# Kernel optimization log

Hardware: AMD Instinct MI355X
Metric: run time of the kernel (lower is better)

## Reference

```python
import jax, jax.numpy as jnp
import numpy as np

B, N, C, H = 2, 1024, 1024, 16
HD = C // H
PAST = 8192
CACHE_BUDGET = 4000
ANCHOR = 512            # anchor_token_count (first-frame tokens preserved)
IMP_W = 0.5             # importance_weight
SCALE = HD ** -0.5


def setup_inputs() -> dict:
    key = jax.random.key(0)
    ks = jax.random.split(key, 8)
    return {
        "x": jax.random.normal(ks[0], (B, N, C), jnp.float32),
        "past_k": jax.random.normal(ks[1], (B, H, PAST, HD), jnp.float32),
        "past_v": jax.random.normal(ks[2], (B, H, PAST, HD), jnp.float32),
        "importance_scores": jax.random.uniform(ks[3], (B, N), dtype=jnp.float32),
        "qkv_w": jax.random.normal(ks[4], (3 * C, C), jnp.float32) * 0.02,
        "qkv_b": jnp.zeros((3 * C,), jnp.float32),
        "proj_w": jax.random.normal(ks[5], (C, C), jnp.float32) * 0.02,
        "proj_b": jnp.zeros((C,), jnp.float32),
    }


def _eviction(k, v, imp):
    # k, v: [B, H, Ntot, D]; imp: [B, N_new]. Hybrid branch of Attention.eviction.
    Bb, Hh, Ntot, D = k.shape
    A = ANCHOR
    Nc = Ntot - A                      # candidates
    keep = CACHE_BUDGET - A            # num_to_keep_from_candidates
    n_old = Nc - N                     # old (past-frame) candidates
    anchor_k, cand_k = k[:, :, :A], k[:, :, A:]
    anchor_v, cand_v = v[:, :, :A], v[:, :, A:]
    # cosine-diversity baseline (F.normalize uses eps=1e-12)
    kn = cand_k / jnp.maximum(jnp.linalg.norm(cand_k, axis=-1, keepdims=True), 1e-12)
    mean_vec = kn.mean(axis=2, keepdims=True)              # [B,H,1,D]
    baseline = jnp.sum(kn * mean_vec, axis=-1)             # [B,H,Nc]
    div_avg = (1.0 - baseline).mean(axis=1)                # [B,Nc]
    old = div_avg[:, :n_old]
    old_n = (old - old.min(axis=-1, keepdims=True)) / (
        old.max(axis=-1, keepdims=True) - old.min(axis=-1, keepdims=True) + 1e-8)
    new_n = (imp - imp.min(axis=-1, keepdims=True)) / (
        imp.max(axis=-1, keepdims=True) - imp.min(axis=-1, keepdims=True) + 1e-8)
    combined = jnp.concatenate([(1.0 - IMP_W) * old_n, IMP_W * new_n], axis=-1)  # [B,Nc]
    _, idx = jax.lax.top_k(combined, keep)
    idx = jnp.sort(idx, axis=-1)                           # [B,keep]
    gidx = jnp.broadcast_to(idx[:, None, :, None], (Bb, Hh, keep, D))
    kept_k = jnp.take_along_axis(cand_k, gidx, axis=2)
    kept_v = jnp.take_along_axis(cand_v, gidx, axis=2)
    return (jnp.concatenate([anchor_k, kept_k], axis=2),
            jnp.concatenate([anchor_v, kept_v], axis=2))


def reference(x, past_k, past_v, importance_scores, qkv_w, qkv_b, proj_w, proj_b):
    # qkv projection -> [3, B, H, N, HD]
    qkv = (x @ qkv_w.T + qkv_b).reshape(B, N, 3, H, HD).transpose(2, 0, 3, 1, 4)
    q, k, v = qkv[0], qkv[1], qkv[2]
    # append to KV cache
    k = jnp.concatenate([past_k, k], axis=2)
    v = jnp.concatenate([past_v, v], axis=2)
    # KV-cache eviction (topk importance + cosine diversity + gather compaction)
    k, v = _eviction(k, v, importance_scores)              # [B,H,CACHE_BUDGET,HD]
    # scaled dot-product attention
    attn = jax.nn.softmax(jnp.einsum('bhqd,bhkd->bhqk', q, k) * SCALE, axis=-1)
    out = jnp.einsum('bhqk,bhkd->bhqd', attn, v)
    out = out.transpose(0, 2, 1, 3).reshape(B, N, C)
    return out @ proj_w.T + proj_b
```

## Files before the change

### kernel.cpp

```cpp
#include <hip/hip_runtime.h>
#include <hip/hip_bf16.h>

typedef unsigned short u16;
typedef unsigned int   u32;
typedef __attribute__((ext_vector_type(8)))  short v8s;
typedef __attribute__((ext_vector_type(4)))  float v4f;
typedef __attribute__((ext_vector_type(16))) float v16f;
typedef __attribute__((ext_vector_type(4)))  u32   v4u;
typedef __attribute__((ext_vector_type(2)))  u32   v2u;

#define B_      2
#define N_      1024
#define C_      1024
#define H_      16
#define BH_     32
#define PAST_   8192
#define BUDGET  4000
#define ANCHOR_ 512
#define NCAND   8704
#define NOLD    7680
#define KEEPN   3488
#define NSPLIT  4
#define QSCALE  0.18033688011112042f

__device__ __forceinline__ u16 f2bf(float f) {
    u32 u = __float_as_uint(f);
    u32 r = u + 0x7fffu + ((u >> 16) & 1u);
    return (u16)(r >> 16);
}
__device__ __forceinline__ float bf2f(u16 h) {
    return __uint_as_float(((u32)h) << 16);
}
__device__ __forceinline__ u32 pk2(float a, float b) {
    __hip_bfloat162 t = __float22bfloat162_rn(float2{a, b});
    u32 r; __builtin_memcpy(&r, &t, 4); return r;
}
__device__ __forceinline__ v8s mk8(u32 a, u32 b, u32 c, u32 d) {
    v4u t; t[0] = a; t[1] = b; t[2] = c; t[3] = d;
    return __builtin_bit_cast(v8s, t);
}

__global__ void prep(const float* __restrict__ x, const float* __restrict__ qw,
                     const float* __restrict__ pw, u16* __restrict__ xcat,
                     u16* __restrict__ wcat, u16* __restrict__ wpbf) {
    const int i = blockIdx.x * 256 + threadIdx.x;
    const int NX = 2048 * 1024, NW = 3072 * 1024;
    if (i < NX) {
        float v = x[i];
        u16 hi = f2bf(v); float lo = v - bf2f(hi);
        const int m = i >> 10, k = i & 1023;
        u16* p = xcat + (size_t)m * 3072 + k;
        p[0] = hi; p[1024] = hi; p[2048] = f2bf(lo);
    } else if (i < NX + NW) {
        const int j = i - NX;
        float v = qw[j];
        u16 hi = f2bf(v); float lo = v - bf2f(hi);
        const int n = j >> 10, k = j & 1023;
        u16* p = wcat + (size_t)n * 3072 + k;
        p[0] = hi; p[1024] = f2bf(lo); p[2048] = hi;
    } else {
        const int j = i - NX - NW;
        wpbf[j] = f2bf(pw[j]);
    }
}

__global__ __launch_bounds__(256) void gemm_qkv(
    const u16* __restrict__ A, const u16* __restrict__ Bm,
    const float* __restrict__ bias,
    u16* __restrict__ Qbf, float* __restrict__ Vnew, float* __restrict__ Kpart) {
    __shared__ u16 As[128 * 72];
    __shared__ u16 Bs[128 * 72];
    const int tid = threadIdx.x;
    const int l = tid & 63, w = tid >> 6;
    const int wm = w >> 1, wn = w & 1;
    const int bid = blockIdx.x;
    int tsel, by, bx, s;
    if (bid < 128)      { tsel = 0; by = bid >> 3; bx = bid & 7; s = 0; }
    else if (bid < 256) { int r = bid - 128; tsel = 2; by = r >> 3; bx = r & 7; s = 0; }
    else                { int r = bid - 256; s = r >> 7; r &= 127; tsel = 1; by = r >> 3; bx = r & 7; }
    const int ks = s * 1024;
    const int nbase = tsel * 1024 + bx * 128;

    v4f acc[4][4];
    #pragma unroll
    for (int a = 0; a < 4; ++a)
        #pragma unroll
        for (int b = 0; b < 4; ++b) { acc[a][b][0]=0.f; acc[a][b][1]=0.f; acc[a][b][2]=0.f; acc[a][b][3]=0.f; }

    const int srow = tid >> 1, shalf = tid & 1;
    const u16* pa = A  + ((size_t)(by * 128 + srow)) * 3072 + ks + shalf * 32;
    const u16* pb = Bm + ((size_t)(nbase + srow))    * 3072 + ks + shalf * 32;
    v4u ar[4], br[4];
    #pragma unroll
    for (int j = 0; j < 4; ++j) { ar[j] = *(const v4u*)(pa + j * 8); br[j] = *(const v4u*)(pb + j * 8); }

    for (int k0 = 0; k0 < 1024; k0 += 64) {
        #pragma unroll
        for (int j = 0; j < 4; ++j) {
            *(v4u*)(&As[srow * 72 + shalf * 32 + j * 8]) = ar[j];
            *(v4u*)(&Bs[srow * 72 + shalf * 32 + j * 8]) = br[j];
        }
        __syncthreads();
        if (k0 + 64 < 1024) {
            #pragma unroll
            for (int j = 0; j < 4; ++j) {
                ar[j] = *(const v4u*)(pa + (k0 + 64) + j * 8);
                br[j] = *(const v4u*)(pb + (k0 + 64) + j * 8);
            }
        }
        #pragma unroll
        for (int kc = 0; kc < 2; ++kc) {
            v8s af[4], bfr[4];
            #pragma unroll
            for (int mt = 0; mt < 4; ++mt)
                af[mt] = *(const v8s*)(&As[(wm * 64 + mt * 16 + (l & 15)) * 72 + kc * 32 + (l >> 4) * 8]);
            #pragma unroll
            for (int nt = 0; nt < 4; ++nt)
                bfr[nt] = *(const v8s*)(&Bs[(wn * 64 + nt * 16 + (l & 15)) * 72 + kc * 32 + (l >> 4) * 8]);
            #pragma unroll
            for (int mt = 0; mt < 4; ++mt)
                #pragma unroll
                for (int nt = 0; nt < 4; ++nt)
                    acc[mt][nt] = __builtin_amdgcn_mfma_f32_16x16x32_bf16(af[mt], bfr[nt], acc[mt][nt], 0, 0, 0);
        }
        __syncthreads();
    }
    #pragma unroll
    for (int nt = 0; nt < 4; ++nt) {
        const int nl = bx * 128 + wn * 64 + nt * 16 + (l & 15);
        const int hh = nl >> 6, dd = nl & 63;
        const float bv = bias[tsel * 1024 + nl];
        #pragma unroll
        for (int mt = 0; mt < 4; ++mt)
            #pragma unroll
            for (int r = 0; r < 4; ++r) {
                const int m = by * 128 + wm * 64 + mt * 16 + (l >> 4) * 4 + r;
                const int bb = m >> 10, nn = m & 1023;
                const size_t o = (((size_t)(bb * 16 + hh)) * 1024 + nn) * 64 + dd;
                if (tsel == 0)      Qbf[o] = f2bf((acc[mt][nt][r] + bv) * QSCALE);
                else if (tsel == 2) Vnew[o] = acc[mt][nt][r] + bv;
                else                Kpart[(size_t)s * 2097152 + o] = acc[mt][nt][r] + (s == 0 ? bv : 0.f);
            }
    }
}

__global__ void kred(float* __restrict__ Kp) {
    const size_t i = ((size_t)blockIdx.x * 256 + threadIdx.x) * 4;
    v4f a = *(const v4f*)(Kp + i);
    v4f b = *(const v4f*)(Kp + 2097152 + i);
    v4f c = *(const v4f*)(Kp + 4194304 + i);
    #pragma unroll
    for (int e = 0; e < 4; ++e) a[e] = (a[e] + b[e]) + c[e];
    *(v4f*)(Kp + i) = a;
}

__global__ __launch_bounds__(256) void kmean(const float* __restrict__ past_k,
                                             const float* __restrict__ Knew,
                                             float* __restrict__ part) {
    __shared__ float Asum[4][64];
    const int blk = blockIdx.x, tid = threadIdx.x;
    const int bh = blk / 34, seg = blk % 34;
    const int l = tid & 63, w = tid >> 6;
    const int rr = l >> 4, dd = l & 15;
    v4f acc; acc[0]=0.f; acc[1]=0.f; acc[2]=0.f; acc[3]=0.f;
    const int base = seg * 256 + w * 64;
    for (int q4 = 0; q4 < 64; q4 += 4) {
        const int i = base + q4 + rr;
        const float* rp = (i < NOLD)
            ? past_k + (((size_t)bh * PAST_) + ANCHOR_ + i) * 64
            : Knew   + (((size_t)bh * N_) + (i - NOLD)) * 64;
        v4f v = *(const v4f*)(rp + dd * 4);
        float ss = v[0]*v[0] + v[1]*v[1] + v[2]*v[2] + v[3]*v[3];
        ss += __shfl_xor(ss, 1); ss += __shfl_xor(ss, 2);
        ss += __shfl_xor(ss, 4); ss += __shfl_xor(ss, 8);
        const float rn = 1.0f / fmaxf(sqrtf(ss), 1e-12f);
        acc[0] += v[0]*rn; acc[1] += v[1]*rn; acc[2] += v[2]*rn; acc[3] += v[3]*rn;
    }
    #pragma unroll
    for (int e = 0; e < 4; ++e) { acc[e] += __shfl_xor(acc[e], 16); acc[e] += __shfl_xor(acc[e], 32); }
    if (l < 16) *(v4f*)(&Asum[w][dd * 4]) = acc;
    __syncthreads();
    if (tid < 64) {
        float s = Asum[0][tid] + Asum[1][tid] + Asum[2][tid] + Asum[3][tid];
        part[((size_t)seg * BH_ + bh) * 64 + tid] = s;
    }
}

__global__ void kmr(const float* __restrict__ part, float* __restrict__ msum) {
    const int i = blockIdx.x * 256 + threadIdx.x;
    if (i < 2048) {
        float s = 0.f;
        for (int g = 0; g < 34; ++g) s += part[(size_t)g * 2048 + i];
        msum[i] = s;
    }
}

__global__ __launch_bounds__(256) void kdiv(const float* __restrict__ past_k,
                                            const float* __restrict__ msum,
                                            float* __restrict__ divavg) {
    __shared__ float MV[1024];
    const int blk = blockIdx.x, tid = threadIdx.x;
    const int b = blk / 240, ib = blk % 240;
    for (int j = tid; j < 1024; j += 256) MV[j] = msum[(size_t)b * 1024 + j] / 8704.0f;
    __syncthreads();
    const int l = tid & 63, w = tid >> 6;
    const int rr = l >> 4, dd = l & 15;
    for (int ii = 0; ii < 8; ++ii) {
        const int i = ib * 32 + w * 8 + ii;
        float accv = 0.f;
        #pragma unroll
        for (int hq = 0; hq < 4; ++hq) {
            const int h = hq * 4 + rr;
            const v4f v  = *(const v4f*)(past_k + (((size_t)(b * 16 + h)) * PAST_ + ANCHOR_ + i) * 64 + dd * 4);
            const v4f mv = *(const v4f*)(&MV[h * 64 + dd * 4]);
            float ss = v[0]*v[0] + v[1]*v[1] + v[2]*v[2] + v[3]*v[3];
            float dp = v[0]*mv[0] + v[1]*mv[1] + v[2]*mv[2] + v[3]*mv[3];
            ss += __shfl_xor(ss, 1); dp += __shfl_xor(dp, 1);
            ss += __shfl_xor(ss, 2); dp += __shfl_xor(dp, 2);
            ss += __shfl_xor(ss, 4); dp += __shfl_xor(dp, 4);
            ss += __shfl_xor(ss, 8); dp += __shfl_xor(dp, 8);
            accv += 1.0f - dp / fmaxf(sqrtf(ss), 1e-12f);
        }
        accv += __shfl_xor(accv, 16); accv += __shfl_xor(accv, 32);
        if (l == 0) divavg[(size_t)b * NOLD + i] = accv / 16.0f;
    }
}

__global__ __launch_bounds__(256) void kselect(const float* __restrict__ divavg,
                                               const float* __restrict__ imp,
                                               int* __restrict__ keep) {
    __shared__ float comb[NCAND];
    __shared__ float red[16];
    __shared__ u32 scnt[2][4];
    __shared__ u32 sg[257], se[257];
    const int b = blockIdx.x, tid = threadIdx.x;
    const int l = tid & 63, w = tid >> 6;

    float mn = 1e30f, mx = -1e30f;
    for (int i = tid; i < NOLD; i += 256) { float v = divavg[b * NOLD + i]; mn = fminf(mn, v); mx = fmaxf(mx, v); }
    #pragma unroll
    for (int d = 1; d < 64; d <<= 1) { mn = fminf(mn, __shfl_xor(mn, d)); mx = fmaxf(mx, __shfl_xor(mx, d)); }
    if (l == 0) { red[w] = mn; red[4 + w] = mx; }
    float mn2 = 1e30f, mx2 = -1e30f;
    for (int i = tid; i < N_; i += 256) { float v = imp[b * N_ + i]; mn2 = fminf(mn2, v); mx2 = fmaxf(mx2, v); }
    #pragma unroll
    for (int d = 1; d < 64; d <<= 1) { mn2 = fminf(mn2, __shfl_xor(mn2, d)); mx2 = fmaxf(mx2, __shfl_xor(mx2, d)); }
    if (l == 0) { red[8 + w] = mn2; red[12 + w] = mx2; }
    __syncthreads();
    const float omin = fminf(fminf(red[0], red[1]), fminf(red[2], red[3]));
    const float omax = fmaxf(fmaxf(red[4], red[5]), fmaxf(red[6], red[7]));
    const float imin = fminf(fminf(red[8], red[9]), fminf(red[10], red[11]));
    const float imax = fmaxf(fmaxf(red[12], red[13]), fmaxf(red[14], red[15]));
    const float oden = omax - omin + 1e-8f, iden = imax - imin + 1e-8f;
    for (int i = tid; i < NCAND; i += 256)
        comb[i] = (i < NOLD) ? 0.5f * ((divavg[b * NOLD + i] - omin) / oden)
                             : 0.5f * ((imp[b * N_ + i - NOLD] - imin) / iden);
    __syncthreads();
    u32 fu[34];
    const int i0 = tid * 34;
    #pragma unroll
    for (int j = 0; j < 34; ++j) fu[j] = __float_as_uint(comb[i0 + j]);
    u32 lo = 0, hi = 0x3F000000u;
    int it = 0;
    while (lo < hi) {
        const u32 mid = lo + ((hi - lo) >> 1);
        u32 c = 0;
        #pragma unroll
        for (int j = 0; j < 34; ++j) c += (fu[j] > mid) ? 1u : 0u;
        c += __shfl_xor(c, 1); c += __shfl_xor(c, 2); c += __shfl_xor(c, 4);
        c += __shfl_xor(c, 8); c += __shfl_xor(c, 16); c += __shfl_xor(c, 32);
        if (l == 0) scnt[it & 1][w] = c;
        __syncthreads();
        const u32 total = scnt[it & 1][0] + scnt[it & 1][1] + scnt[it & 1][2] + scnt[it & 1][3];
        if (total < KEEPN) hi = mid; else lo = mid + 1;
        ++it;
    }
    const u32 tau = lo;
    u32 ng = 0, ne = 0;
    #pragma unroll
    for (int j = 0; j < 34; ++j) { ng += (fu[j] > tau); ne += (fu[j] == tau); }
    sg[tid + 1] = ng; se[tid + 1] = ne;
    __syncthreads();
    if (tid == 0) { sg[0] = 0; se[0] = 0; for (int t = 1; t <= 256; ++t) { sg[t] += sg[t - 1]; se[t] += se[t - 1]; } }
    __syncthreads();
    const u32 need = KEEPN - sg[256];
    u32 g = sg[tid], e = se[tid];
    #pragma unroll
    for (int j = 0; j < 34; ++j) {
        const u32 u = fu[j];
        const bool kg = u > tau;
        const bool ke = (u == tau) && (e < need);
        if (kg || ke) keep[b * KEEPN + (g + (e < need ? e : need))] = 512 + i0 + j;
        g += kg ? 1u : 0u; e += (u == tau) ? 1u : 0u;
    }
}

__global__ __launch_bounds__(256) void kgather(const float* __restrict__ past_k,
    const float* __restrict__ past_v, const float* __restrict__ Knew,
    const float* __restrict__ Vnew, const int* __restrict__ keep,
    u16* __restrict__ Kg, u16* __restrict__ VTg) {
    __shared__ float VL[64][65];
    const int blk = blockIdx.x, tid = threadIdx.x;
    const int bh = blk / 63, jb = blk % 63;
    const int b = bh >> 4;
    const int jj = tid >> 2, cc = tid & 3;
    const int j = jb * 64 + jj;
    if (j < BUDGET) {
        const int row = (j < ANCHOR_) ? j : keep[b * KEEPN + (j - ANCHOR_)];
        const float *ks, *vs;
        if (row < PAST_) { size_t o = ((size_t)bh * PAST_ + row) * 64; ks = past_k + o; vs = past_v + o; }
        else             { size_t o = ((size_t)bh * N_ + (row - PAST_)) * 64; ks = Knew + o; vs = Vnew + o; }
        union { u16 h[16]; v4u v[2]; } pk_;
        #pragma unroll
        for (int q4 = 0; q4 < 4; ++q4) {
            v4f kv = *(const v4f*)(ks + cc * 16 + q4 * 4);
            v4f vv = *(const v4f*)(vs + cc * 16 + q4 * 4);
            #pragma unroll
            for (int e = 0; e < 4; ++e) {
                pk_.h[q4 * 4 + e] = f2bf(kv[e]);
                VL[jj][cc * 16 + q4 * 4 + e] = vv[e];
            }
        }
        v4u* kout = (v4u*)(Kg + ((size_t)bh * BUDGET + j) * 64 + cc * 16);
        kout[0] = pk_.v[0]; kout[1] = pk_.v[1];
    }
    __syncthreads();
    const int d = tid >> 2, c4 = tid & 3;
    const int jc = c4 * 16;
    if (jb * 64 + jc < BUDGET) {
        union { u16 h[16]; v4u v[2]; } pv_;
        #pragma unroll
        for (int t2 = 0; t2 < 16; ++t2) pv_.h[t2] = f2bf(VL[jc + t2][d]);
        v4u* vout = (v4u*)(VTg + ((size_t)bh * 64 + d) * BUDGET + jb * 64 + jc);
        vout[0] = pv_.v[0]; vout[1] = pv_.v[1];
    }
}

__global__ __launch_bounds__(128, 3) void attn(const u16* __restrict__ Qbf,
    const u16* __restrict__ Kg, const u16* __restrict__ VTg,
    float* __restrict__ Opart, float* __restrict__ Mpart, float* __restrict__ Lpart) {
    __shared__ u16 Ks[2][32 * 72];
    __shared__ u16 Vs[2][64 * 40];
    const int tid = threadIdx.x;
    const int l = tid & 63, w = tid >> 6;
    const int G = l >> 5, lq = l & 31;
    const int bid = ((blockIdx.x & 7) << 8) | (blockIdx.x >> 3);
    const int bh = bid >> 6, rem = bid & 63;
    const int split = rem & 3, qblk = rem >> 2;
    const int q = qblk * 64 + w * 32 + lq;
    const int t0 = split * 32;
    const int t1 = (split == 3) ? 125 : (t0 + 32);

    v8s Qf[4];
    const v8s* qp = (const v8s*)(Qbf + ((size_t)(bh * 1024 + q)) * 64);
    #pragma unroll
    for (int c = 0; c < 4; ++c) Qf[c] = qp[c * 2 + G];

    v16f o0, o1;
    #pragma unroll
    for (int e = 0; e < 16; ++e) { o0[e] = 0.f; o1[e] = 0.f; }
    float mrun = -1e30f, lrun = 0.f;

    const int krow = tid >> 2, kc = tid & 3;
    const int vrow = tid >> 1, vc = tid & 1;
    const u16* kbase = Kg + ((size_t)bh * BUDGET + krow) * 64 + kc * 16;
    const u16* vbase = VTg + ((size_t)bh * 64 + vrow) * BUDGET + vc * 16;
    v4u kr0 = *(const v4u*)(kbase + (size_t)t0 * 2048);
    v4u kr1 = *(const v4u*)(kbase + (size_t)t0 * 2048 + 8);
    v4u vr0 = *(const v4u*)(vbase + t0 * 32);
    v4u vr1 = *(const v4u*)(vbase + t0 * 32 + 8);
    int cur = 0;

    for (int t = t0; t < t1; ++t) {
        *(v4u*)(&Ks[cur][krow * 72 + kc * 16])     = kr0;
        *(v4u*)(&Ks[cur][krow * 72 + kc * 16 + 8]) = kr1;
        *(v4u*)(&Vs[cur][vrow * 40 + vc * 16])     = vr0;
        *(v4u*)(&Vs[cur][vrow * 40 + vc * 16 + 8]) = vr1;
        if (t + 1 < t1) {
            kr0 = *(const v4u*)(kbase + (size_t)(t + 1) * 2048);
            kr1 = *(const v4u*)(kbase + (size_t)(t + 1) * 2048 + 8);
            vr0 = *(const v4u*)(vbase + (t + 1) * 32);
            vr1 = *(const v4u*)(vbase + (t + 1) * 32 + 8);
        }
        __syncthreads();
        v16f s;
        #pragma unroll
        for (int e = 0; e < 16; ++e) s[e] = 0.f;
        v8s kf[4];
        #pragma unroll
        for (int c = 0; c < 4; ++c) kf[c] = *(const v8s*)(&Ks[cur][lq * 72 + c * 16 + G * 8]);
        __builtin_amdgcn_s_setprio(1);
        #pragma unroll
        for (int c = 0; c < 4; ++c)
            s = __builtin_amdgcn_mfma_f32_32x32x16_bf16(kf[c], Qf[c], s, 0, 0, 0);
        __builtin_amdgcn_s_setprio(0);
        float m0 = fmaxf(s[0], s[1]),  m1 = fmaxf(s[2], s[3]),  m2 = fmaxf(s[4], s[5]),  m3 = fmaxf(s[6], s[7]);
        float m4 = fmaxf(s[8], s[9]),  m5 = fmaxf(s[10], s[11]), m6 = fmaxf(s[12], s[13]), m7 = fmaxf(s[14], s[15]);
        float mt = fmaxf(fmaxf(fmaxf(m0, m1), fmaxf(m2, m3)), fmaxf(fmaxf(m4, m5), fmaxf(m6, m7)));
        mt = fmaxf(mt, __shfl_xor(mt, 32));
        if (__any(mt > mrun + 8.0f)) {
            const float mnew = fmaxf(mrun, mt);
            const float alpha = exp2f(mrun - mnew);
            #pragma unroll
            for (int e = 0; e < 16; ++e) { o0[e] *= alpha; o1[e] *= alpha; }
            lrun *= alpha;
            mrun = mnew;
        }
        float p[16];
        #pragma unroll
        for (int e = 0; e < 16; ++e) p[e] = exp2f(s[e] - mrun);
        float l0 = (p[0] + p[1]) + (p[2] + p[3]), l1 = (p[4] + p[5]) + (p[6] + p[7]);
        float l2 = (p[8] + p[9]) + (p[10] + p[11]), l3 = (p[12] + p[13]) + (p[14] + p[15]);
        lrun += (l0 + l1) + (l2 + l3);
        u32 dP[8];
        #pragma unroll
        for (int e = 0; e < 8; ++e) dP[e] = pk2(p[2 * e], p[2 * e + 1]);
        auto r02 = __builtin_amdgcn_permlane32_swap(dP[0], dP[2], false, false);
        auto r13 = __builtin_amdgcn_permlane32_swap(dP[1], dP[3], false, false);
        auto r46 = __builtin_amdgcn_permlane32_swap(dP[4], dP[6], false, false);
        auto r57 = __builtin_amdgcn_permlane32_swap(dP[5], dP[7], false, false);
        const v8s P0 = mk8(r02[0], r13[0], r02[1], r13[1]);
        const v8s P1 = mk8(r46[0], r57[0], r46[1], r57[1]);
        v8s va0 = *(const v8s*)(&Vs[cur][lq * 40 + G * 8]);
        v8s vb0 = *(const v8s*)(&Vs[cur][(32 + lq) * 40 + G * 8]);
        v8s va1 = *(const v8s*)(&Vs[cur][lq * 40 + 16 + G * 8]);
        v8s vb1 = *(const v8s*)(&Vs[cur][(32 + lq) * 40 + 16 + G * 8]);
        __builtin_amdgcn_s_setprio(1);
        o0 = __builtin_amdgcn_mfma_f32_32x32x16_bf16(va0, P0, o0, 0, 0, 0);
        o1 = __builtin_amdgcn_mfma_f32_32x32x16_bf16(vb0, P0, o1, 0, 0, 0);
        o0 = __builtin_amdgcn_mfma_f32_32x32x16_bf16(va1, P1, o0, 0, 0, 0);
        o1 = __builtin_amdgcn_mfma_f32_32x32x16_bf16(vb1, P1, o1, 0, 0, 0);
        __builtin_amdgcn_s_setprio(0);
        cur ^= 1;
    }
    const float ltot = lrun + __shfl_xor(lrun, 32);
    const size_t base = (((size_t)(split * 32 + bh)) * 1024 + q) * 64;
    #pragma unroll
    for (int c = 0; c < 2; ++c) {
        #pragma unroll
        for (int rq = 0; rq < 4; ++rq) {
            v4f v;
            #pragma unroll
            for (int e = 0; e < 4; ++e) v[e] = (c ? o1[4 * rq + e] : o0[4 * rq + e]);
            *(v4f*)(Opart + base + 32 * c + 8 * rq + 4 * G) = v;
        }
    }
    if (G == 0) {
        Mpart[(size_t)(split * 32 + bh) * 1024 + q] = mrun;
        Lpart[(size_t)(split * 32 + bh) * 1024 + q] = ltot;
    }
}

__global__ void kmerge(const float* __restrict__ Op, const float* __restrict__ Mp,
                       const float* __restrict__ Lp, u16* __restrict__ attnbf) {
    const int idx = blockIdx.x * 256 + threadIdx.x;
    const int dq = idx & 15, q = (idx >> 4) & 1023, bh = idx >> 14;
    float m[NSPLIT], li[NSPLIT];
    #pragma unroll
    for (int s = 0; s < NSPLIT; ++s) {
        m[s]  = Mp[(size_t)(s * 32 + bh) * 1024 + q];
        li[s] = Lp[(size_t)(s * 32 + bh) * 1024 + q];
    }
    const float M = fmaxf(fmaxf(m[0], m[1]), fmaxf(m[2], m[3]));
    float ww[NSPLIT]; float den = 0.f;
    #pragma unroll
    for (int s = 0; s < NSPLIT; ++s) { ww[s] = exp2f(m[s] - M); den += ww[s] * li[s]; }
    const float rden = 1.0f / den;
    v4f acc; acc[0]=0.f; acc[1]=0.f; acc[2]=0.f; acc[3]=0.f;
    #pragma unroll
    for (int s = 0; s < NSPLIT; ++s) {
        const v4f a = *(const v4f*)(Op + ((((size_t)(s * 32 + bh)) * 1024 + q) * 64) + dq * 4);
        #pragma unroll
        for (int e = 0; e < 4; ++e) acc[e] += ww[s] * a[e];
    }
    union { u16 h[4]; v2u v; } r_;
    #pragma unroll
    for (int e = 0; e < 4; ++e) r_.h[e] = f2bf(acc[e] * rden);
    const int bb = bh >> 4, h = bh & 15;
    *(v2u*)(attnbf + ((size_t)(bb * 1024 + q)) * 1024 + h * 64 + dq * 4) = r_.v;
}

__global__ __launch_bounds__(256) void gemm_proj64(
    const u16* __restrict__ A, const u16* __restrict__ Bm,
    const float* __restrict__ bias, float* __restrict__ Cout) {
    __shared__ u16 As[64 * 72];
    __shared__ u16 Bs[64 * 72];
    const int tid = threadIdx.x;
    const int l = tid & 63, w = tid >> 6;
    const int wm = w >> 1, wn = w & 1;
    const int by = blockIdx.x >> 4, bx = blockIdx.x & 15;
    v4f acc[2][2];
    #pragma unroll
    for (int a = 0; a < 2; ++a)
        #pragma unroll
        for (int b = 0; b < 2; ++b) { acc[a][b][0]=0.f; acc[a][b][1]=0.f; acc[a][b][2]=0.f; acc[a][b][3]=0.f; }

    const int srow = tid >> 2, sq = tid & 3;
    const u16* pa = A  + ((size_t)(by * 64 + srow)) * 1024 + sq * 16;
    const u16* pb = Bm + ((size_t)(bx * 64 + srow)) * 1024 + sq * 16;
    v4u ar[2], br[2];
    #pragma unroll
    for (int j = 0; j < 2; ++j) { ar[j] = *(const v4u*)(pa + j * 8); br[j] = *(const v4u*)(pb + j * 8); }

    for (int k0 = 0; k0 < 1024; k0 += 64) {
        #pragma unroll
        for (int j = 0; j < 2; ++j) {
            *(v4u*)(&As[srow * 72 + sq * 16 + j * 8]) = ar[j];
            *(v4u*)(&Bs[srow * 72 + sq * 16 + j * 8]) = br[j];
        }
        __syncthreads();
        if (k0 + 64 < 1024) {
            #pragma unroll
            for (int j = 0; j < 2; ++j) {
                ar[j] = *(const v4u*)(pa + (k0 + 64) + j * 8);
                br[j] = *(const v4u*)(pb + (k0 + 64) + j * 8);
            }
        }
        #pragma unroll
        for (int kc = 0; kc < 2; ++kc) {
            v8s af[2], bfr[2];
            #pragma unroll
            for (int mt = 0; mt < 2; ++mt)
                af[mt] = *(const v8s*)(&As[(wm * 32 + mt * 16 + (l & 15)) * 72 + kc * 32 + (l >> 4) * 8]);
            #pragma unroll
            for (int nt = 0; nt < 2; ++nt)
                bfr[nt] = *(const v8s*)(&Bs[(wn * 32 + nt * 16 + (l & 15)) * 72 + kc * 32 + (l >> 4) * 8]);
            #pragma unroll
            for (int mt = 0; mt < 2; ++mt)
                #pragma unroll
                for (int nt = 0; nt < 2; ++nt)
                    acc[mt][nt] = __builtin_amdgcn_mfma_f32_16x16x32_bf16(af[mt], bfr[nt], acc[mt][nt], 0, 0, 0);
        }
        __syncthreads();
    }
    #pragma unroll
    for (int nt = 0; nt < 2; ++nt) {
        const int n = bx * 64 + wn * 32 + nt * 16 + (l & 15);
        const float bv = bias[n];
        #pragma unroll
        for (int mt = 0; mt < 2; ++mt)
            #pragma unroll
            for (int r = 0; r < 4; ++r) {
                const int m = by * 64 + wm * 32 + mt * 16 + (l >> 4) * 4 + r;
                Cout[(size_t)m * 1024 + n] = acc[mt][nt][r] + bv;
            }
    }
}

extern "C" void kernel_launch(void* const* d_in, const int* in_sizes, int n_in,
                              void* d_out, int out_size, void* d_ws, size_t ws_size,
                              hipStream_t stream) {
    const float* x      = (const float*)d_in[0];
    const float* past_k = (const float*)d_in[1];
    const float* past_v = (const float*)d_in[2];
    const float* imp    = (const float*)d_in[3];
    const float* qkv_w  = (const float*)d_in[4];
    const float* qkv_b  = (const float*)d_in[5];
    const float* proj_w = (const float*)d_in[6];
    const float* proj_b = (const float*)d_in[7];
    float* out = (float*)d_out;
    char* ws = (char*)d_ws;

    const size_t o_kg    = 0;
    const size_t o_vtg   = 16384000;
    const size_t o_xcat  = 0;
    const size_t o_wcat  = 12582912;
    const size_t o_abf   = 0;
    const size_t o_wproj = 32768000;
    const size_t o_qbf   = 34865152;
    const size_t o_opart = 39059456;
    const size_t o_kpart = 39059456;
    const size_t o_vnew  = 64225280;
    const size_t o_part  = 72613888;
    const size_t o_msum  = 72892416;
    const size_t o_div   = 72900608;
    const size_t o_keep  = 72962048;
    const size_t o_mpart = 72989952;
    const size_t o_lpart = 73514240;
    const size_t total   = 74038528;
    if (ws_size < total) return;

    u16*   xcat  = (u16*)(ws + o_xcat);
    u16*   wcat  = (u16*)(ws + o_wcat);
    u16*   Kg    = (u16*)(ws + o_kg);
    u16*   VTg   = (u16*)(ws + o_vtg);
    u16*   wproj = (u16*)(ws + o_wproj);
    u16*   Qbf   = (u16*)(ws + o_qbf);
    float* Kpart = (float*)(ws + o_kpart);
    float* Knew  = Kpart;
    float* Vnew  = (float*)(ws + o_vnew);
    float* Opart = (float*)(ws + o_opart);
    float* part  = (float*)(ws + o_part);
    float* msum  = (float*)(ws + o_msum);
    float* divavg= (float*)(ws + o_div);
    int*   keep  = (int*)(ws + o_keep);
    float* Mpart = (float*)(ws + o_mpart);
    float* Lpart = (float*)(ws + o_lpart);
    u16*   attnbf= (u16*)(ws + o_abf);

    prep<<<24576, 256, 0, stream>>>(x, qkv_w, proj_w, xcat, wcat, wproj);
    gemm_qkv<<<640, 256, 0, stream>>>(xcat, wcat, qkv_b, Qbf, Vnew, Kpart);
    kred<<<2048, 256, 0, stream>>>(Kpart);
    kmean<<<1088, 256, 0, stream>>>(past_k, Knew, part);
    kmr<<<8, 256, 0, stream>>>(part, msum);
    kdiv<<<480, 256, 0, stream>>>(past_k, msum, divavg);
    kselect<<<2, 256, 0, stream>>>(divavg, imp, keep);
    kgather<<<2016, 256, 0, stream>>>(past_k, past_v, Knew, Vnew, keep, Kg, VTg);
    attn<<<2048, 128, 0, stream>>>(Qbf, Kg, VTg, Opart, Mpart, Lpart);
    kmerge<<<2048, 256, 0, stream>>>(Opart, Mpart, Lpart, attnbf);
    gemm_proj64<<<512, 256, 0, stream>>>(attnbf, wproj, proj_b, out);
}
```

Measured before the change: 240.5 us.

## Load K/V fragments directly from global into registers, drop LDS staging

The attention kernel now uses single-wave blocks (64 threads, twice the grid) and reads each lane's K and V MFMA fragments straight from global memory instead of staging tiles through double-buffered shared memory. K fragments for the next tile are prefetched in registers, and the block-wide barriers and setprio hints are removed. This avoids LDS traffic and synchronisation, but loses the sharing of K/V tiles between two waves of one block, so global/L2 reads double. The per-lane global loads are also less coalesced, especially the strided V rows.

```diff
diff --git a/kernel.cpp b/kernel.cpp
--- a/kernel.cpp
+++ b/kernel.cpp
@@ -336,18 +336,15 @@
     }
 }
 
-__global__ __launch_bounds__(128, 3) void attn(const u16* __restrict__ Qbf,
+__global__ __launch_bounds__(64, 3) void attn(const u16* __restrict__ Qbf,
     const u16* __restrict__ Kg, const u16* __restrict__ VTg,
     float* __restrict__ Opart, float* __restrict__ Mpart, float* __restrict__ Lpart) {
-    __shared__ u16 Ks[2][32 * 72];
-    __shared__ u16 Vs[2][64 * 40];
-    const int tid = threadIdx.x;
-    const int l = tid & 63, w = tid >> 6;
+    const int l = threadIdx.x;
     const int G = l >> 5, lq = l & 31;
-    const int bid = ((blockIdx.x & 7) << 8) | (blockIdx.x >> 3);
-    const int bh = bid >> 6, rem = bid & 63;
+    const int bid = ((blockIdx.x & 7) << 9) | (blockIdx.x >> 3);
+    const int bh = bid >> 7, rem = bid & 127;
     const int split = rem & 3, qblk = rem >> 2;
-    const int q = qblk * 64 + w * 32 + lq;
+    const int q = qblk * 32 + lq;
     const int t0 = split * 32;
     const int t1 = (split == 3) ? 125 : (t0 + 32);
 
@@ -361,39 +358,31 @@
     for (int e = 0; e < 16; ++e) { o0[e] = 0.f; o1[e] = 0.f; }
     float mrun = -1e30f, lrun = 0.f;
 
-    const int krow = tid >> 2, kc = tid & 3;
-    const int vrow = tid >> 1, vc = tid & 1;
-    const u16* kbase = Kg + ((size_t)bh * BUDGET + krow) * 64 + kc * 16;
-    const u16* vbase = VTg + ((size_t)bh * 64 + vrow) * BUDGET + vc * 16;
-    v4u kr0 = *(const v4u*)(kbase + (size_t)t0 * 2048);
-    v4u kr1 = *(const v4u*)(kbase + (size_t)t0 * 2048 + 8);
-    v4u vr0 = *(const v4u*)(vbase + t0 * 32);
-    v4u vr1 = *(const v4u*)(vbase + t0 * 32 + 8);
-    int cur = 0;
+    const u16* kp = Kg  + (((size_t)bh * BUDGET + (size_t)t0 * 32 + lq) * 64) + G * 8;
+    const u16* vp = VTg + (((size_t)bh * 64 + lq) * BUDGET) + (size_t)t0 * 32 + G * 8;
+
+    v8s kf0 = *(const v8s*)(kp);
+    v8s kf1 = *(const v8s*)(kp + 16);
+    v8s kf2 = *(const v8s*)(kp + 32);
+    v8s kf3 = *(const v8s*)(kp + 48);
 
     for (int t = t0; t < t1; ++t) {
-        *(v4u*)(&Ks[cur][krow * 72 + kc * 16])     = kr0;
-        *(v4u*)(&Ks[cur][krow * 72 + kc * 16 + 8]) = kr1;
-        *(v4u*)(&Vs[cur][vrow * 40 + vc * 16])     = vr0;
-        *(v4u*)(&Vs[cur][vrow * 40 + vc * 16 + 8]) = vr1;
-        if (t + 1 < t1) {
-            kr0 = *(const v4u*)(kbase + (size_t)(t + 1) * 2048);
-            kr1 = *(const v4u*)(kbase + (size_t)(t + 1) * 2048 + 8);
-            vr0 = *(const v4u*)(vbase + (t + 1) * 32);
-            vr1 = *(const v4u*)(vbase + (t + 1) * 32 + 8);
-        }
-        __syncthreads();
+        v8s va0 = *(const v8s*)(vp);
+        v8s va1 = *(const v8s*)(vp + 16);
+        v8s vb0 = *(const v8s*)(vp + (size_t)32 * BUDGET);
+        v8s vb1 = *(const v8s*)(vp + (size_t)32 * BUDGET + 16);
+        const size_t koff = (t + 1 < t1) ? 2048 : 0;
+        v8s nk0 = *(const v8s*)(kp + koff);
+        v8s nk1 = *(const v8s*)(kp + koff + 16);
+        v8s nk2 = *(const v8s*)(kp + koff + 32);
+        v8s nk3 = *(const v8s*)(kp + koff + 48);
         v16f s;
         #pragma unroll
         for (int e = 0; e < 16; ++e) s[e] = 0.f;
-        v8s kf[4];
-        #pragma unroll
-        for (int c = 0; c < 4; ++c) kf[c] = *(const v8s*)(&Ks[cur][lq * 72 + c * 16 + G * 8]);
-        __builtin_amdgcn_s_setprio(1);
-        #pragma unroll
-        for (int c = 0; c < 4; ++c)
-            s = __builtin_amdgcn_mfma_f32_32x32x16_bf16(kf[c], Qf[c], s, 0, 0, 0);
-        __builtin_amdgcn_s_setprio(0);
+        s = __builtin_amdgcn_mfma_f32_32x32x16_bf16(kf0, Qf[0], s, 0, 0, 0);
+        s = __builtin_amdgcn_mfma_f32_32x32x16_bf16(kf1, Qf[1], s, 0, 0, 0);
+        s = __builtin_amdgcn_mfma_f32_32x32x16_bf16(kf2, Qf[2], s, 0, 0, 0);
+        s = __builtin_amdgcn_mfma_f32_32x32x16_bf16(kf3, Qf[3], s, 0, 0, 0);
         float m0 = fmaxf(s[0], s[1]),  m1 = fmaxf(s[2], s[3]),  m2 = fmaxf(s[4], s[5]),  m3 = fmaxf(s[6], s[7]);
         float m4 = fmaxf(s[8], s[9]),  m5 = fmaxf(s[10], s[11]), m6 = fmaxf(s[12], s[13]), m7 = fmaxf(s[14], s[15]);
         float mt = fmaxf(fmaxf(fmaxf(m0, m1), fmaxf(m2, m3)), fmaxf(fmaxf(m4, m5), fmaxf(m6, m7)));
@@ -421,17 +410,12 @@
         auto r57 = __builtin_amdgcn_permlane32_swap(dP[5], dP[7], false, false);
         const v8s P0 = mk8(r02[0], r13[0], r02[1], r13[1]);
         const v8s P1 = mk8(r46[0], r57[0], r46[1], r57[1]);
-        v8s va0 = *(const v8s*)(&Vs[cur][lq * 40 + G * 8]);
-        v8s vb0 = *(const v8s*)(&Vs[cur][(32 + lq) * 40 + G * 8]);
-        v8s va1 = *(const v8s*)(&Vs[cur][lq * 40 + 16 + G * 8]);
-        v8s vb1 = *(const v8s*)(&Vs[cur][(32 + lq) * 40 + 16 + G * 8]);
-        __builtin_amdgcn_s_setprio(1);
         o0 = __builtin_amdgcn_mfma_f32_32x32x16_bf16(va0, P0, o0, 0, 0, 0);
         o1 = __builtin_amdgcn_mfma_f32_32x32x16_bf16(vb0, P0, o1, 0, 0, 0);
         o0 = __builtin_amdgcn_mfma_f32_32x32x16_bf16(va1, P1, o0, 0, 0, 0);
         o1 = __builtin_amdgcn_mfma_f32_32x32x16_bf16(vb1, P1, o1, 0, 0, 0);
-        __builtin_amdgcn_s_setprio(0);
-        cur ^= 1;
+        kf0 = nk0; kf1 = nk1; kf2 = nk2; kf3 = nk3;
+        kp += 2048; vp += 32;
     }
     const float ltot = lrun + __shfl_xor(lrun, 32);
     const size_t base = (((size_t)(split * 32 + bh)) * 1024 + q) * 64;
@@ -606,7 +590,7 @@
     kdiv<<<480, 256, 0, stream>>>(past_k, msum, divavg);
     kselect<<<2, 256, 0, stream>>>(divavg, imp, keep);
     kgather<<<2016, 256, 0, stream>>>(past_k, past_v, Knew, Vnew, keep, Kg, VTg);
-    attn<<<2048, 128, 0, stream>>>(Qbf, Kg, VTg, Opart, Mpart, Lpart);
+    attn<<<4096, 64, 0, stream>>>(Qbf, Kg, VTg, Opart, Mpart, Lpart);
     kmerge<<<2048, 256, 0, stream>>>(Opart, Mpart, Lpart, attnbf);
     gemm_proj64<<<512, 256, 0, stream>>>(attnbf, wproj, proj_b, out);
 }
```

Measured after the change: 269.3 us. 12.0% more time.

## Use direct global-to-LDS loads with XOR swizzle in QKV GEMM and fuse K split reduction

Applied to the files above, without the earlier changes.

The QKV GEMM now stages A/B tiles with global_load_lds straight into unpadded, XOR-swizzled shared memory instead of going through registers with a 72-stride padded layout. In exchange it drops the register prefetch of the next tile, so global loads no longer overlap with MFMA work. Separately, the kred kernel that summed the three K split-K partials is removed. The sum is recomputed on the fly in kmean and kgather, saving a launch and a full write/read pass at the cost of extra partial reads there.

```diff
diff --git a/kernel.cpp b/kernel.cpp
--- a/kernel.cpp
+++ b/kernel.cpp
@@ -21,6 +21,7 @@
 #define NOLD    7680
 #define KEEPN   3488
 #define NSPLIT  4
+#define KSLICE  2097152
 #define QSCALE  0.18033688011112042f
 
 __device__ __forceinline__ u16 f2bf(float f) {
@@ -38,6 +39,10 @@
 __device__ __forceinline__ v8s mk8(u32 a, u32 b, u32 c, u32 d) {
     v4u t; t[0] = a; t[1] = b; t[2] = c; t[3] = d;
     return __builtin_bit_cast(v8s, t);
+}
+__device__ __forceinline__ void glds16(const u16* g, u16* l) {
+    __builtin_amdgcn_global_load_lds((const __attribute__((address_space(1))) u32*)g,
+                                     (__attribute__((address_space(3))) u32*)l, 16, 0, 0);
 }
 
 __global__ void prep(const float* __restrict__ x, const float* __restrict__ qw,
@@ -68,8 +73,8 @@
     const u16* __restrict__ A, const u16* __restrict__ Bm,
     const float* __restrict__ bias,
     u16* __restrict__ Qbf, float* __restrict__ Vnew, float* __restrict__ Kpart) {
-    __shared__ u16 As[128 * 72];
-    __shared__ u16 Bs[128 * 72];
+    __shared__ u16 As[128 * 64];
+    __shared__ u16 Bs[128 * 64];
     const int tid = threadIdx.x;
     const int l = tid & 63, w = tid >> 6;
     const int wm = w >> 1, wn = w & 1;
@@ -87,43 +92,40 @@
         #pragma unroll
         for (int b = 0; b < 4; ++b) { acc[a][b][0]=0.f; acc[a][b][1]=0.f; acc[a][b][2]=0.f; acc[a][b][3]=0.f; }
 
-    const int srow = tid >> 1, shalf = tid & 1;
-    const u16* pa = A  + ((size_t)(by * 128 + srow)) * 3072 + ks + shalf * 32;
-    const u16* pb = Bm + ((size_t)(nbase + srow))    * 3072 + ks + shalf * 32;
-    v4u ar[4], br[4];
-    #pragma unroll
-    for (int j = 0; j < 4; ++j) { ar[j] = *(const v4u*)(pa + j * 8); br[j] = *(const v4u*)(pb + j * 8); }
+    const int lrow = l >> 3;
+    const int lgr  = (l & 7) ^ lrow;
+    const u16* pa = A  + ((size_t)(by * 128 + w * 32 + lrow)) * 3072 + ks + lgr * 8;
+    const u16* pb = Bm + ((size_t)(nbase + w * 32 + lrow))    * 3072 + ks + lgr * 8;
 
     for (int k0 = 0; k0 < 1024; k0 += 64) {
+        if (k0) __syncthreads();
         #pragma unroll
         for (int j = 0; j < 4; ++j) {
-            *(v4u*)(&As[srow * 72 + shalf * 32 + j * 8]) = ar[j];
-            *(v4u*)(&Bs[srow * 72 + shalf * 32 + j * 8]) = br[j];
+            glds16(pa + j * 24576 + k0, &As[w * 2048 + j * 512]);
+            glds16(pb + j * 24576 + k0, &Bs[w * 2048 + j * 512]);
         }
         __syncthreads();
-        if (k0 + 64 < 1024) {
-            #pragma unroll
-            for (int j = 0; j < 4; ++j) {
-                ar[j] = *(const v4u*)(pa + (k0 + 64) + j * 8);
-                br[j] = *(const v4u*)(pb + (k0 + 64) + j * 8);
-            }
-        }
         #pragma unroll
         for (int kc = 0; kc < 2; ++kc) {
             v8s af[4], bfr[4];
             #pragma unroll
-            for (int mt = 0; mt < 4; ++mt)
-                af[mt] = *(const v8s*)(&As[(wm * 64 + mt * 16 + (l & 15)) * 72 + kc * 32 + (l >> 4) * 8]);
-            #pragma unroll
-            for (int nt = 0; nt < 4; ++nt)
-                bfr[nt] = *(const v8s*)(&Bs[(wn * 64 + nt * 16 + (l & 15)) * 72 + kc * 32 + (l >> 4) * 8]);
+            for (int mt = 0; mt < 4; ++mt) {
+                const int R = wm * 64 + mt * 16 + (l & 15);
+                const int g = (kc * 4 + (l >> 4)) ^ (R & 7);
+                af[mt] = *(const v8s*)(&As[R * 64 + g * 8]);
+            }
+            #pragma unroll
+            for (int nt = 0; nt < 4; ++nt) {
+                const int R = wn * 64 + nt * 16 + (l & 15);
+                const int g = (kc * 4 + (l >> 4)) ^ (R & 7);
+                bfr[nt] = *(const v8s*)(&Bs[R * 64 + g * 8]);
+            }
             #pragma unroll
             for (int mt = 0; mt < 4; ++mt)
                 #pragma unroll
                 for (int nt = 0; nt < 4; ++nt)
                     acc[mt][nt] = __builtin_amdgcn_mfma_f32_16x16x32_bf16(af[mt], bfr[nt], acc[mt][nt], 0, 0, 0);
         }
-        __syncthreads();
     }
     #pragma unroll
     for (int nt = 0; nt < 4; ++nt) {
@@ -139,23 +141,13 @@
                 const size_t o = (((size_t)(bb * 16 + hh)) * 1024 + nn) * 64 + dd;
                 if (tsel == 0)      Qbf[o] = f2bf((acc[mt][nt][r] + bv) * QSCALE);
                 else if (tsel == 2) Vnew[o] = acc[mt][nt][r] + bv;
-                else                Kpart[(size_t)s * 2097152 + o] = acc[mt][nt][r] + (s == 0 ? bv : 0.f);
+                else                Kpart[(size_t)s * KSLICE + o] = acc[mt][nt][r] + (s == 0 ? bv : 0.f);
             }
     }
 }
 
-__global__ void kred(float* __restrict__ Kp) {
-    const size_t i = ((size_t)blockIdx.x * 256 + threadIdx.x) * 4;
-    v4f a = *(const v4f*)(Kp + i);
-    v4f b = *(const v4f*)(Kp + 2097152 + i);
-    v4f c = *(const v4f*)(Kp + 4194304 + i);
-    #pragma unroll
-    for (int e = 0; e < 4; ++e) a[e] = (a[e] + b[e]) + c[e];
-    *(v4f*)(Kp + i) = a;
-}
-
 __global__ __launch_bounds__(256) void kmean(const float* __restrict__ past_k,
-                                             const float* __restrict__ Knew,
+                                             const float* __restrict__ Kp,
                                              float* __restrict__ part) {
     __shared__ float Asum[4][64];
     const int blk = blockIdx.x, tid = threadIdx.x;
@@ -166,10 +158,17 @@
     const int base = seg * 256 + w * 64;
     for (int q4 = 0; q4 < 64; q4 += 4) {
         const int i = base + q4 + rr;
-        const float* rp = (i < NOLD)
-            ? past_k + (((size_t)bh * PAST_) + ANCHOR_ + i) * 64
-            : Knew   + (((size_t)bh * N_) + (i - NOLD)) * 64;
-        v4f v = *(const v4f*)(rp + dd * 4);
+        v4f v;
+        if (i < NOLD) {
+            v = *(const v4f*)(past_k + (((size_t)bh * PAST_) + ANCHOR_ + i) * 64 + dd * 4);
+        } else {
+            const float* r0 = Kp + (((size_t)bh * N_) + (i - NOLD)) * 64 + dd * 4;
+            v4f a = *(const v4f*)r0;
+            v4f b = *(const v4f*)(r0 + KSLICE);
+            v4f c = *(const v4f*)(r0 + 2 * KSLICE);
+            #pragma unroll
+            for (int e = 0; e < 4; ++e) v[e] = (a[e] + b[e]) + c[e];
+        }
         float ss = v[0]*v[0] + v[1]*v[1] + v[2]*v[2] + v[3]*v[3];
         ss += __shfl_xor(ss, 1); ss += __shfl_xor(ss, 2);
         ss += __shfl_xor(ss, 4); ss += __shfl_xor(ss, 8);
@@ -296,7 +295,7 @@
 }
 
 __global__ __launch_bounds__(256) void kgather(const float* __restrict__ past_k,
-    const float* __restrict__ past_v, const float* __restrict__ Knew,
+    const float* __restrict__ past_v, const float* __restrict__ Kp,
     const float* __restrict__ Vnew, const int* __restrict__ keep,
     u16* __restrict__ Kg, u16* __restrict__ VTg) {
     __shared__ float VL[64][65];
@@ -307,18 +306,36 @@
     const int j = jb * 64 + jj;
     if (j < BUDGET) {
         const int row = (j < ANCHOR_) ? j : keep[b * KEEPN + (j - ANCHOR_)];
-        const float *ks, *vs;
-        if (row < PAST_) { size_t o = ((size_t)bh * PAST_ + row) * 64; ks = past_k + o; vs = past_v + o; }
-        else             { size_t o = ((size_t)bh * N_ + (row - PAST_)) * 64; ks = Knew + o; vs = Vnew + o; }
         union { u16 h[16]; v4u v[2]; } pk_;
-        #pragma unroll
-        for (int q4 = 0; q4 < 4; ++q4) {
-            v4f kv = *(const v4f*)(ks + cc * 16 + q4 * 4);
-            v4f vv = *(const v4f*)(vs + cc * 16 + q4 * 4);
-            #pragma unroll
-            for (int e = 0; e < 4; ++e) {
-                pk_.h[q4 * 4 + e] = f2bf(kv[e]);
-                VL[jj][cc * 16 + q4 * 4 + e] = vv[e];
+        if (row < PAST_) {
+            const size_t o = ((size_t)bh * PAST_ + row) * 64;
+            const float* ks = past_k + o;
+            const float* vs = past_v + o;
+            #pragma unroll
+            for (int q4 = 0; q4 < 4; ++q4) {
+                v4f kv = *(const v4f*)(ks + cc * 16 + q4 * 4);
+                v4f vv = *(const v4f*)(vs + cc * 16 + q4 * 4);
+                #pragma unroll
+                for (int e = 0; e < 4; ++e) {
+                    pk_.h[q4 * 4 + e] = f2bf(kv[e]);
+                    VL[jj][cc * 16 + q4 * 4 + e] = vv[e];
+                }
+            }
+        } else {
+            const size_t o = ((size_t)bh * N_ + (row - PAST_)) * 64;
+            const float* k0 = Kp + o;
+            const float* vs = Vnew + o;
+            #pragma unroll
+            for (int q4 = 0; q4 < 4; ++q4) {
+                v4f a = *(const v4f*)(k0 + cc * 16 + q4 * 4);
+                v4f bb2 = *(const v4f*)(k0 + KSLICE + cc * 16 + q4 * 4);
+                v4f c = *(const v4f*)(k0 + 2 * KSLICE + cc * 16 + q4 * 4);
+                v4f vv = *(const v4f*)(vs + cc * 16 + q4 * 4);
+                #pragma unroll
+                for (int e = 0; e < 4; ++e) {
+                    pk_.h[q4 * 4 + e] = f2bf((a[e] + bb2[e]) + c[e]);
+                    VL[jj][cc * 16 + q4 * 4 + e] = vv[e];
+                }
             }
         }
         v4u* kout = (v4u*)(Kg + ((size_t)bh * BUDGET + j) * 64 + cc * 16);
@@ -587,7 +604,6 @@
     u16*   wproj = (u16*)(ws + o_wproj);
     u16*   Qbf   = (u16*)(ws + o_qbf);
     float* Kpart = (float*)(ws + o_kpart);
-    float* Knew  = Kpart;
     float* Vnew  = (float*)(ws + o_vnew);
     float* Opart = (float*)(ws + o_opart);
     float* part  = (float*)(ws + o_part);
@@ -600,12 +616,11 @@
 
     prep<<<24576, 256, 0, stream>>>(x, qkv_w, proj_w, xcat, wcat, wproj);
     gemm_qkv<<<640, 256, 0, stream>>>(xcat, wcat, qkv_b, Qbf, Vnew, Kpart);
-    kred<<<2048, 256, 0, stream>>>(Kpart);
-    kmean<<<1088, 256, 0, stream>>>(past_k, Knew, part);
+    kmean<<<1088, 256, 0, stream>>>(past_k, Kpart, part);
     kmr<<<8, 256, 0, stream>>>(part, msum);
     kdiv<<<480, 256, 0, stream>>>(past_k, msum, divavg);
     kselect<<<2, 256, 0, stream>>>(divavg, imp, keep);
-    kgather<<<2016, 256, 0, stream>>>(past_k, past_v, Knew, Vnew, keep, Kg, VTg);
+    kgather<<<2016, 256, 0, stream>>>(past_k, past_v, Kpart, Vnew, keep, Kg, VTg);
     attn<<<2048, 128, 0, stream>>>(Qbf, Kg, VTg, Opart, Mpart, Lpart);
     kmerge<<<2048, 256, 0, stream>>>(Opart, Mpart, Lpart, attnbf);
     gemm_proj64<<<512, 256, 0, stream>>>(attnbf, wproj, proj_b, out);
```

Result: faster. 234.4 us (-2.5%).
